# Optimization experiments

Hardware: AMD Instinct MI355X
Metric: run time of the kernel (lower is better)

## Reference

```python
import jax, jax.numpy as jnp
import numpy as np

H, KVH, HD, D, FF = 16, 4, 128, 2048, 7168
EPS = 1e-5
ROPE_THETA = 10000.0
SCALE_FACTOR, SCALE_GAP = 1.0, 0.7


def rms_norm(x, w):
    v = jnp.mean(jnp.square(x.astype(jnp.float32)), axis=-1, keepdims=True)
    return (x.astype(jnp.float32) * jax.lax.rsqrt(v + EPS)).astype(x.dtype) * w


def apply_rope(x, pos):
    # x: [B,S,h,HD], pos: [S]
    inv = 1.0 / (ROPE_THETA ** (jnp.arange(0, HD, 2, dtype=jnp.float32) / HD))
    ang = pos.astype(jnp.float32)[:, None] * inv[None, :]              # [S,HD/2]
    cos = jnp.concatenate([jnp.cos(ang)] * 2, -1)[None, :, None, :]    # [1,S,1,HD]
    sin = jnp.concatenate([jnp.sin(ang)] * 2, -1)[None, :, None, :]
    x1, x2 = jnp.split(x, 2, axis=-1)
    rot = jnp.concatenate([-x2, x1], axis=-1)
    return x * cos + rot * sin


def attention(x, q_w, k_w, v_w, o_w):
    B, S, _ = x.shape
    pos = jnp.arange(S)
    q = apply_rope((x @ q_w.T).reshape(B, S, H, HD), pos)
    k = apply_rope((x @ k_w.T).reshape(B, S, KVH, HD), pos)
    v = (x @ v_w.T).reshape(B, S, KVH, HD)
    rep = H // KVH
    k = jnp.repeat(k, rep, axis=2)   # [B,S,H,HD]
    v = jnp.repeat(v, rep, axis=2)
    scores = jnp.einsum('bqhd,bkhd->bhqk', q, k) / np.sqrt(HD).astype(np.float32)
    causal = jnp.tril(jnp.ones((S, S), dtype=bool))
    scores = jnp.where(causal[None, None], scores, jnp.finfo(scores.dtype).min)
    probs = jax.nn.softmax(scores, axis=-1)
    out = jnp.einsum('bhqk,bkhd->bqhd', probs, v).reshape(B, S, H * HD)
    return out @ o_w.T


def mlp(x, gate_w, up_w, down_w):
    return (jax.nn.silu(x @ gate_w.T) * (x @ up_w.T)) @ down_w.T


def setup_inputs() -> dict:
    key = jax.random.key(0)
    ks = jax.random.split(key, 12)
    B, S = 2, 2048
    w = lambda k, shp: (jax.random.normal(k, shp, dtype=jnp.float32) * 0.02)
    return {
        'hidden_states': jax.random.normal(ks[0], (B, S, D), dtype=jnp.float32),
        'topk_mask': jax.random.randint(ks[1], (B, S), 0, 2) > 0,
        'topk_scores': jax.random.uniform(ks[2], (B, S), dtype=jnp.float32),
        'ln1_w': jnp.ones((D,), jnp.float32),
        'ln2_w': jnp.ones((D,), jnp.float32),
        'q_w': w(ks[3], (H * HD, D)),
        'k_w': w(ks[4], (KVH * HD, D)),
        'v_w': w(ks[5], (KVH * HD, D)),
        'o_w': w(ks[6], (D, H * HD)),
        'gate_w': w(ks[7], (FF, D)),
        'up_w': w(ks[8], (FF, D)),
        'down_w': w(ks[9], (D, FF)),
    }


def reference(hidden_states, topk_mask, topk_scores, ln1_w, ln2_w,
              q_w, k_w, v_w, o_w, gate_w, up_w, down_w):
    # attention block
    h = hidden_states + attention(rms_norm(hidden_states, ln1_w), q_w, k_w, v_w, o_w)
    # MoD top-k masked MLP: only selected tokens go through MLP, scaled, scattered back
    m = mlp(rms_norm(h, ln2_w), gate_w, up_w, down_w)
    scores = 0.5 * SCALE_FACTOR + (topk_scores - 0.5) * SCALE_GAP
    upd = jnp.where(topk_mask[..., None], m * scores[..., None], 0.0)
    return h + upd
```

## Files before the change

### kernel.cpp

```cpp
#include <hip/hip_runtime.h>
#include <stdint.h>

#define SEQ    2048
#define DMODEL 2048
#define NTOK   4096
#define NHEAD  16
#define NKVH   4
#define HDIM   128
#define FFDIM  7168
#define FFH    3584
#define QKVS   3072

typedef __bf16 bf16x8 __attribute__((ext_vector_type(8)));
typedef float  floatx4 __attribute__((ext_vector_type(4)));

__device__ __forceinline__ float bf2f(unsigned short u) {
  union { unsigned int i; float f; } v; v.i = ((unsigned int)u) << 16; return v.f;
}
__device__ __forceinline__ unsigned short f2bf(float f) {
  union { float f; unsigned int u; } v; v.f = f;
  unsigned int r = (v.u + 0x7FFFu + ((v.u >> 16) & 1u)) >> 16;
  return (unsigned short)r;
}
__device__ __forceinline__ uint4 ld8f32(const float* p) {
  float4 a = *(const float4*)p, b = *(const float4*)(p + 4);
  union { unsigned short s[8]; uint4 v; } o;
  o.s[0] = f2bf(a.x); o.s[1] = f2bf(a.y); o.s[2] = f2bf(a.z); o.s[3] = f2bf(a.w);
  o.s[4] = f2bf(b.x); o.s[5] = f2bf(b.y); o.s[6] = f2bf(b.z); o.s[7] = f2bf(b.w);
  return o.v;
}

__device__ __forceinline__ void gload16(const unsigned short* g, unsigned short* l) {
  __builtin_amdgcn_global_load_lds(
      (const __attribute__((address_space(1))) unsigned int*)g,
      (__attribute__((address_space(3))) unsigned int*)l, 16, 0, 0);
}

__global__ __launch_bounds__(256) void wconv(const float* __restrict__ s,
                                             unsigned short* __restrict__ d) {
  const size_t i = ((size_t)blockIdx.x * 256 + threadIdx.x) * 8;
  *(uint4*)(d + i) = ld8f32(s + i);
}

__global__ __launch_bounds__(256) void wconv_dn(const float* __restrict__ s,
                                                unsigned short* __restrict__ d, int koff) {
  const int r = blockIdx.x;
  const float* sp = s + (size_t)r * FFDIM + koff;
  unsigned short* dp = d + (size_t)r * FFH;
  for (int c = threadIdx.x * 8; c < FFH; c += 2048)
    *(uint4*)(dp + c) = ld8f32(sp + c);
}

#define GEMM_CORE(Aptr, Wptr, KK)                                                \
  __shared__ __align__(16) unsigned short As[128 * 32];                          \
  __shared__ __align__(16) unsigned short Bs[128 * 32];                          \
  const int tid  = threadIdx.x;                                                  \
  const int wave = tid >> 6, lane = tid & 63;                                    \
  const int quad = lane >> 4, l16 = lane & 15;                                   \
  const int row0 = blockIdx.y * 128, col0 = blockIdx.x * 128;                    \
  const int wm = (wave >> 1) * 64, wn = (wave & 1) * 64;                         \
  const floatx4 z = {0.f, 0.f, 0.f, 0.f};                                       \
  floatx4 acc[4][4];                                                             \
  _Pragma("unroll") for (int i = 0; i < 4; ++i)                                  \
  _Pragma("unroll") for (int j = 0; j < 4; ++j) acc[i][j] = z;                   \
  const int ar0 = tid >> 2, ac0 = (tid & 3) << 3;                                \
  unsigned short* lA0 = &As[wave * 512];                                         \
  unsigned short* lA1 = &As[2048 + wave * 512];                                  \
  unsigned short* lB0 = &Bs[wave * 512];                                         \
  unsigned short* lB1 = &Bs[2048 + wave * 512];                                  \
  const unsigned short* gA0 = (Aptr) + (size_t)(row0 + ar0) * (KK) + ac0;        \
  const unsigned short* gA1 = (Aptr) + (size_t)(row0 + 64 + ar0) * (KK) + ac0;   \
  const unsigned short* gB0 = (Wptr) + (size_t)(col0 + ar0) * (KK) + ac0;        \
  const unsigned short* gB1 = (Wptr) + (size_t)(col0 + 64 + ar0) * (KK) + ac0;   \
  for (int k0 = 0; k0 < (KK); k0 += 32) {                                        \
    gload16(gA0 + k0, lA0);                                                      \
    gload16(gA1 + k0, lA1);                                                      \
    gload16(gB0 + k0, lB0);                                                      \
    gload16(gB1 + k0, lB1);                                                      \
    __syncthreads();                                                             \
    bf16x8 af[4], bfr[4];                                                        \
    _Pragma("unroll") for (int i = 0; i < 4; ++i) {                              \
      af[i]  = *(const bf16x8*)&As[(wm + i * 16 + l16) * 32 + quad * 8];         \
      bfr[i] = *(const bf16x8*)&Bs[(wn + i * 16 + l16) * 32 + quad * 8];         \
    }                                                                            \
    _Pragma("unroll") for (int mi = 0; mi < 4; ++mi)                             \
    _Pragma("unroll") for (int ni = 0; ni < 4; ++ni)                             \
      acc[mi][ni] =                                                              \
          __builtin_amdgcn_mfma_f32_16x16x32_bf16(af[mi], bfr[ni], acc[mi][ni], 0, 0, 0); \
    __syncthreads();                                                             \
  }

__global__ __launch_bounds__(256) void gemm_bt(
    const unsigned short* __restrict__ A, const unsigned short* __restrict__ W,
    unsigned short* __restrict__ C, int N, int K) {
  GEMM_CORE(A, W, K)
#pragma unroll
  for (int mi = 0; mi < 4; ++mi) {
    const int r = row0 + wm + mi * 16 + quad * 4;
#pragma unroll
    for (int ni = 0; ni < 4; ++ni) {
      const int cc = col0 + wn + ni * 16 + l16;
#pragma unroll
      for (int reg = 0; reg < 4; ++reg)
        C[(size_t)(r + reg) * N + cc] = f2bf(acc[mi][ni][reg]);
    }
  }
}

__global__ __launch_bounds__(256) void gemm_o_res(
    const unsigned short* __restrict__ A, const unsigned short* __restrict__ W,
    const float* __restrict__ X, float* __restrict__ Hout) {
  GEMM_CORE(A, W, DMODEL)
#pragma unroll
  for (int mi = 0; mi < 4; ++mi) {
    const int r = row0 + wm + mi * 16 + quad * 4;
#pragma unroll
    for (int ni = 0; ni < 4; ++ni) {
      const int cc = col0 + wn + ni * 16 + l16;
#pragma unroll
      for (int reg = 0; reg < 4; ++reg) {
        const size_t idx = (size_t)(r + reg) * DMODEL + cc;
        Hout[idx] = X[idx] + acc[mi][ni][reg];
      }
    }
  }
}

__global__ __launch_bounds__(256) void gemm_down_add(
    const unsigned short* __restrict__ A, const unsigned short* __restrict__ W,
    const float* __restrict__ ts, const int* __restrict__ tok_of,
    const int* __restrict__ cnt, float* __restrict__ out) {
  const int nrow = *cnt;
  if (blockIdx.y * 128 >= nrow) return;
  GEMM_CORE(A, W, FFH)
#pragma unroll
  for (int mi = 0; mi < 4; ++mi) {
    const int r = row0 + wm + mi * 16 + quad * 4;
#pragma unroll
    for (int ni = 0; ni < 4; ++ni) {
      const int cc = col0 + wn + ni * 16 + l16;
#pragma unroll
      for (int reg = 0; reg < 4; ++reg) {
        const int rr = r + reg;
        if (rr < nrow) {
          const int tok = tok_of[rr];
          const float scv = 0.5f + (ts[tok] - 0.5f) * 0.7f;
          out[(size_t)tok * DMODEL + cc] += acc[mi][ni][reg] * scv;
        }
      }
    }
  }
}

__global__ __launch_bounds__(256) void gemm_gateup(
    const unsigned short* __restrict__ A, const unsigned short* __restrict__ G,
    const unsigned short* __restrict__ U, const int* __restrict__ cnt,
    unsigned short* __restrict__ act) {
  if (blockIdx.y * 128 >= *cnt) return;
  __shared__ __align__(16) unsigned short As[128 * 32];
  __shared__ __align__(16) unsigned short Gs[64 * 32];
  __shared__ __align__(16) unsigned short Us[64 * 32];
  const int tid  = threadIdx.x;
  const int wave = tid >> 6, lane = tid & 63;
  const int quad = lane >> 4, l16 = lane & 15;
  const int row0 = blockIdx.y * 128, colg = blockIdx.x * 64;
  const int wm = (wave >> 1) * 64, wn = (wave & 1) * 32;

  const floatx4 z = {0.f, 0.f, 0.f, 0.f};
  floatx4 accG[4][2], accU[4][2];
#pragma unroll
  for (int i = 0; i < 4; ++i)
#pragma unroll
    for (int j = 0; j < 2; ++j) { accG[i][j] = z; accU[i][j] = z; }

  const int ar0 = tid >> 2, ac0 = (tid & 3) << 3;
  unsigned short* lA0 = &As[wave * 512];
  unsigned short* lA1 = &As[2048 + wave * 512];
  unsigned short* lG  = &Gs[wave * 512];
  unsigned short* lU  = &Us[wave * 512];
  const unsigned short* gA0 = A + (size_t)(row0 + ar0) * DMODEL + ac0;
  const unsigned short* gA1 = A + (size_t)(row0 + 64 + ar0) * DMODEL + ac0;
  const unsigned short* gG  = G + (size_t)(colg + ar0) * DMODEL + ac0;
  const unsigned short* gU  = U + (size_t)(colg + ar0) * DMODEL + ac0;

  for (int k0 = 0; k0 < DMODEL; k0 += 32) {
    gload16(gA0 + k0, lA0);
    gload16(gA1 + k0, lA1);
    gload16(gG + k0, lG);
    gload16(gU + k0, lU);
    __syncthreads();
    bf16x8 af[4], bg[2], bu[2];
#pragma unroll
    for (int i = 0; i < 4; ++i)
      af[i] = *(const bf16x8*)&As[(wm + i * 16 + l16) * 32 + quad * 8];
#pragma unroll
    for (int j = 0; j < 2; ++j) {
      bg[j] = *(const bf16x8*)&Gs[(wn + j * 16 + l16) * 32 + quad * 8];
      bu[j] = *(const bf16x8*)&Us[(wn + j * 16 + l16) * 32 + quad * 8];
    }
#pragma unroll
    for (int mi = 0; mi < 4; ++mi)
#pragma unroll
      for (int ni = 0; ni < 2; ++ni) {
        accG[mi][ni] = __builtin_amdgcn_mfma_f32_16x16x32_bf16(af[mi], bg[ni], accG[mi][ni], 0, 0, 0);
        accU[mi][ni] = __builtin_amdgcn_mfma_f32_16x16x32_bf16(af[mi], bu[ni], accU[mi][ni], 0, 0, 0);
      }
    __syncthreads();
  }
#pragma unroll
  for (int mi = 0; mi < 4; ++mi) {
    const int r = row0 + wm + mi * 16 + quad * 4;
#pragma unroll
    for (int ni = 0; ni < 2; ++ni) {
      const int cc = colg + wn + ni * 16 + l16;
#pragma unroll
      for (int reg = 0; reg < 4; ++reg) {
        const float g = accG[mi][ni][reg];
        const float u = accU[mi][ni][reg];
        const float s = g / (1.f + __expf(-g));
        act[(size_t)(r + reg) * FFH + cc] = f2bf(s * u);
      }
    }
  }
}

__global__ __launch_bounds__(256) void rmsnorm_f32(
    const float* __restrict__ x, const float* __restrict__ w,
    unsigned short* __restrict__ out) {
  __shared__ float red[4];
  const int row = blockIdx.x, tid = threadIdx.x;
  const int lane = tid & 63, wave = tid >> 6;
  const size_t base = (size_t)row * DMODEL + tid * 8;
  float4 a = *(const float4*)(x + base);
  float4 b = *(const float4*)(x + base + 4);
  float v[8] = {a.x, a.y, a.z, a.w, b.x, b.y, b.z, b.w};
  float ss = 0.f;
#pragma unroll
  for (int j = 0; j < 8; ++j) ss += v[j] * v[j];
#pragma unroll
  for (int off = 32; off; off >>= 1) ss += __shfl_xor(ss, off);
  if (lane == 0) red[wave] = ss;
  __syncthreads();
  const float tot = red[0] + red[1] + red[2] + red[3];
  const float rms = rsqrtf(tot * (1.f / (float)DMODEL) + 1e-5f);
  float4 wa = *(const float4*)(w + tid * 8);
  float4 wb = *(const float4*)(w + tid * 8 + 4);
  const float wv[8] = {wa.x, wa.y, wa.z, wa.w, wb.x, wb.y, wb.z, wb.w};
  unsigned short o[8];
#pragma unroll
  for (int j = 0; j < 8; ++j) o[j] = f2bf(v[j] * rms * wv[j]);
  *(uint4*)(out + base) = *(const uint4*)o;
}

__global__ void zero_cnt(int* cnt) { *cnt = 0; }

__global__ __launch_bounds__(256) void rms_gather(
    const float* __restrict__ x, const float* __restrict__ w,
    const int* __restrict__ mask, int* __restrict__ cnt,
    int* __restrict__ tok_of, unsigned short* __restrict__ xc) {
  const int row = blockIdx.x;
  if (!mask[row]) return;
  __shared__ float red[4];
  __shared__ int ppos;
  const int tid = threadIdx.x, lane = tid & 63, wave = tid >> 6;
  if (tid == 0) { const int p = atomicAdd(cnt, 1); ppos = p; tok_of[p] = row; }
  const size_t base = (size_t)row * DMODEL + tid * 8;
  float4 a = *(const float4*)(x + base);
  float4 b = *(const float4*)(x + base + 4);
  float v[8] = {a.x, a.y, a.z, a.w, b.x, b.y, b.z, b.w};
  float ss = 0.f;
#pragma unroll
  for (int j = 0; j < 8; ++j) ss += v[j] * v[j];
#pragma unroll
  for (int off = 32; off; off >>= 1) ss += __shfl_xor(ss, off);
  if (lane == 0) red[wave] = ss;
  __syncthreads();
  const float tot = red[0] + red[1] + red[2] + red[3];
  const float rms = rsqrtf(tot * (1.f / (float)DMODEL) + 1e-5f);
  float4 wa = *(const float4*)(w + tid * 8);
  float4 wb = *(const float4*)(w + tid * 8 + 4);
  const float wv[8] = {wa.x, wa.y, wa.z, wa.w, wb.x, wb.y, wb.z, wb.w};
  unsigned short o[8];
#pragma unroll
  for (int j = 0; j < 8; ++j) o[j] = f2bf(v[j] * rms * wv[j]);
  *(uint4*)(xc + (size_t)ppos * DMODEL + tid * 8) = *(const uint4*)o;
}

__global__ __launch_bounds__(256) void rope_k(unsigned short* __restrict__ buf,
                                              int nh, int rstride) {
  const int t = blockIdx.x;
  const int s = t & (SEQ - 1);
  const int d = threadIdx.x & 63;
  const float inv = __expf((float)d * -0.14391156843712787f);
  float sn, cs;
  __sincosf((float)s * inv, &sn, &cs);
  const int npair = nh * 64;
  for (int idx = threadIdx.x; idx < npair; idx += 256) {
    const int hh = idx >> 6;
    unsigned short* p = buf + (size_t)t * rstride + hh * 128 + d;
    const float x1 = bf2f(p[0]), x2 = bf2f(p[64]);
    p[0]  = f2bf(x1 * cs - x2 * sn);
    p[64] = f2bf(x2 * cs + x1 * sn);
  }
}

__global__ __launch_bounds__(512, 2) void attn(
    const unsigned short* __restrict__ QKV,
    unsigned short* __restrict__ O) {
  __shared__ __align__(16) unsigned short Ks[64 * 136];
  __shared__ __align__(16) unsigned short Vt[128 * 80];
  __shared__ __align__(16) unsigned short Ps[8][16 * 88];
  const int h = blockIdx.x, b = blockIdx.z;
  const int qtL = blockIdx.y, qtH = 15 - qtL;
  const int kvh = h >> 2;
  const int tid = threadIdx.x, wave = tid >> 6, lane = tid & 63;
  const int quad = lane >> 4, l16 = lane & 15;
  const int wloH = qtH * 128 + wave * 16;
  const int wloL = qtL * 128 + wave * 16;
  const int qrH = wloH + quad * 4, qrL = wloL + quad * 4;
  const float sscale = 0.08838834764831845f;

  bf16x8 qfH[4], qfL[4];
  {
    const unsigned short* qpH =
        QKV + (size_t)(b * SEQ + wloH + l16) * QKVS + h * HDIM + quad * 8;
    const unsigned short* qpL =
        QKV + (size_t)(b * SEQ + wloL + l16) * QKVS + h * HDIM + quad * 8;
#pragma unroll
    for (int c = 0; c < 4; ++c) {
      qfH[c] = *(const bf16x8*)(qpH + 32 * c);
      qfL[c] = *(const bf16x8*)(qpL + 32 * c);
    }
  }
  const floatx4 z = {0.f, 0.f, 0.f, 0.f};
  floatx4 accH[8], accL[8];
#pragma unroll
  for (int i = 0; i < 8; ++i) { accH[i] = z; accL[i] = z; }
  float mH[4], lH[4], mL[4], lL[4];
#pragma unroll
  for (int r = 0; r < 4; ++r) { mH[r] = -1e30f; lH[r] = 0.f; mL[r] = -1e30f; lL[r] = 0.f; }

  const int sr = tid >> 4, scol = (tid & 15) * 8;
  const unsigned short* kvb = QKV + (size_t)(b * SEQ) * QKVS + kvh * HDIM;
  uint4 kreg[2], vreg[2];

  auto LOADT = [&](int t0) {
#pragma unroll
    for (int it = 0; it < 2; ++it) {
      const int r = sr + it * 32;
      kreg[it] = *(const uint4*)(kvb + (size_t)(t0 + r) * QKVS + 2048 + scol);
      vreg[it] = *(const uint4*)(kvb + (size_t)(t0 + r) * QKVS + 2560 + scol);
    }
  };
  auto STORET = [&]() {
#pragma unroll
    for (int it = 0; it < 2; ++it) {
      const int r = sr + it * 32;
      *(uint4*)&Ks[r * 136 + scol] = kreg[it];
      const unsigned short* dv = (const unsigned short*)&vreg[it];
      const int tb = r >> 3, pos = r & 7;
#pragma unroll
      for (int j = 0; j < 8; ++j) {
        const int d = scol + j;
        const int sb = tb ^ ((d >> 3) & 7);
        Vt[d * 80 + sb * 8 + pos] = dv[j];
      }
    }
  };

  auto COMPUTE = [&](const bf16x8* qf, floatx4* accO, float* mrow, float* lrow,
                     int qrowC, int wlo, int t0) {
    floatx4 sc[4];
    __builtin_amdgcn_s_setprio(1);
#pragma unroll
    for (int ni = 0; ni < 4; ++ni) {
      floatx4 s = z;
#pragma unroll
      for (int c = 0; c < 4; ++c) {
        bf16x8 kf = *(const bf16x8*)&Ks[(ni * 16 + l16) * 136 + c * 32 + quad * 8];
        s = __builtin_amdgcn_mfma_f32_16x16x32_bf16(qf[c], kf, s, 0, 0, 0);
      }
      sc[ni] = s;
    }
    __builtin_amdgcn_s_setprio(0);

    if (t0 + 63 > wlo) {
#pragma unroll
      for (int ni = 0; ni < 4; ++ni) {
        const int kcol = t0 + ni * 16 + l16;
#pragma unroll
        for (int reg = 0; reg < 4; ++reg) {
          const float vv = sc[ni][reg] * sscale;
          sc[ni][reg] = (kcol > qrowC + reg) ? -1e30f : vv;
        }
      }
    } else {
#pragma unroll
      for (int ni = 0; ni < 4; ++ni)
#pragma unroll
        for (int reg = 0; reg < 4; ++reg) sc[ni][reg] *= sscale;
    }

    float mx[4];
#pragma unroll
    for (int reg = 0; reg < 4; ++reg) {
      float m0 = fmaxf(fmaxf(sc[0][reg], sc[1][reg]), fmaxf(sc[2][reg], sc[3][reg]));
#pragma unroll
      for (int off = 1; off < 16; off <<= 1) m0 = fmaxf(m0, __shfl_xor(m0, off));
      mx[reg] = m0;
    }
    const bool grow = (mx[0] > mrow[0] + 8.f) || (mx[1] > mrow[1] + 8.f) ||
                      (mx[2] > mrow[2] + 8.f) || (mx[3] > mrow[3] + 8.f);
    if (__any(grow)) {
#pragma unroll
      for (int reg = 0; reg < 4; ++reg) {
        const float mnew = fmaxf(mrow[reg], mx[reg]);
        const float alpha = __expf(mrow[reg] - mnew);
        mrow[reg] = mnew;
        lrow[reg] *= alpha;
#pragma unroll
        for (int nd = 0; nd < 8; ++nd) accO[nd][reg] *= alpha;
      }
    }
#pragma unroll
    for (int reg = 0; reg < 4; ++reg) {
      float rs = 0.f;
#pragma unroll
      for (int ni = 0; ni < 4; ++ni) {
        const float p = __expf(sc[ni][reg] - mrow[reg]);
        sc[ni][reg] = p;
        rs += p;
      }
#pragma unroll
      for (int off = 1; off < 16; off <<= 1) rs += __shfl_xor(rs, off);
      lrow[reg] += rs;
    }
#pragma unroll
    for (int ni = 0; ni < 4; ++ni)
#pragma unroll
      for (int reg = 0; reg < 4; ++reg)
        Ps[wave][(quad * 4 + reg) * 88 + ni * 16 + l16] = f2bf(sc[ni][reg]);
    const bf16x8 pa0 = *(const bf16x8*)&Ps[wave][l16 * 88 + quad * 8];
    const bf16x8 pa1 = *(const bf16x8*)&Ps[wave][l16 * 88 + 32 + quad * 8];
    __builtin_amdgcn_s_setprio(1);
#pragma unroll
    for (int nd = 0; nd < 8; ++nd) {
      const int d = nd * 16 + l16;
      const int f = (d >> 3) & 7;
      bf16x8 v0 = *(const bf16x8*)&Vt[d * 80 + ((quad ^ f) << 3)];
      bf16x8 v1 = *(const bf16x8*)&Vt[d * 80 + (((quad + 4) ^ f) << 3)];
      accO[nd] = __builtin_amdgcn_mfma_f32_16x16x32_bf16(pa0, v0, accO[nd], 0, 0, 0);
      accO[nd] = __builtin_amdgcn_mfma_f32_16x16x32_bf16(pa1, v1, accO[nd], 0, 0, 0);
    }
    __builtin_amdgcn_s_setprio(0);
  };

  const int ntL = 2 * qtL + 2, ntH = 2 * qtH + 2;
  LOADT(0);
  STORET();
  __syncthreads();

  for (int ti = 0; ti < ntH; ++ti) {
    const int t0 = ti * 64;
    const bool more = (ti + 1 < ntH);
    if (more) LOADT(t0 + 64);

    if (t0 <= wloH + 15) COMPUTE(qfH, accH, mH, lH, qrH, wloH, t0);
    if (ti < ntL && t0 <= wloL + 15) COMPUTE(qfL, accL, mL, lL, qrL, wloL, t0);

    __syncthreads();
    if (more) {
      STORET();
      __syncthreads();
    }
  }
#pragma unroll
  for (int nd = 0; nd < 8; ++nd)
#pragma unroll
    for (int reg = 0; reg < 4; ++reg) {
      const float oH = accH[nd][reg] / lH[reg];
      O[(size_t)(b * SEQ + qrH + reg) * (NHEAD * HDIM) + h * HDIM + nd * 16 + l16] = f2bf(oH);
      const float oL = accL[nd][reg] / lL[reg];
      O[(size_t)(b * SEQ + qrL + reg) * (NHEAD * HDIM) + h * HDIM + nd * 16 + l16] = f2bf(oL);
    }
}

extern "C" void kernel_launch(void* const* d_in, const int* in_sizes, int n_in,
                              void* d_out, int out_size, void* d_ws, size_t ws_size,
                              hipStream_t stream) {
  (void)in_sizes; (void)n_in; (void)out_size; (void)ws_size;
  const float* x    = (const float*)d_in[0];
  const int*   mask = (const int*)d_in[1];
  const float* ts   = (const float*)d_in[2];
  const float* ln1  = (const float*)d_in[3];
  const float* ln2  = (const float*)d_in[4];
  const float* q_w  = (const float*)d_in[5];
  const float* k_w  = (const float*)d_in[6];
  const float* v_w  = (const float*)d_in[7];
  const float* o_w  = (const float*)d_in[8];
  const float* g_w  = (const float*)d_in[9];
  const float* u_w  = (const float*)d_in[10];
  const float* dn_w = (const float*)d_in[11];
  float* out = (float*)d_out;

  char* ws = (char*)d_ws;
  unsigned short* xn    = (unsigned short*)(ws + 0);
  unsigned short* qkv   = (unsigned short*)(ws + 16777216);
  unsigned short* wqkv  = (unsigned short*)(ws + 41943040);
  unsigned short* attno = (unsigned short*)(ws + 41943040);
  unsigned short* wo    = (unsigned short*)(ws + 58720256);
  unsigned short* xc    = (unsigned short*)(ws + 0);
  unsigned short* wg    = (unsigned short*)(ws + 16777216);
  unsigned short* wu    = (unsigned short*)(ws + 31457280);
  unsigned short* wdn   = (unsigned short*)(ws + 16777216);
  unsigned short* act   = (unsigned short*)(ws + 46137344);
  int*            cnt   = (int*)           (ws + 75497472);
  int*            tok_of= (int*)           (ws + 75501568);

  wconv<<<2048, 256, 0, stream>>>(q_w, wqkv);
  wconv<<<512,  256, 0, stream>>>(k_w, wqkv + (size_t)2048 * DMODEL);
  wconv<<<512,  256, 0, stream>>>(v_w, wqkv + (size_t)2560 * DMODEL);
  wconv<<<2048, 256, 0, stream>>>(o_w, wo);

  rmsnorm_f32<<<NTOK, 256, 0, stream>>>(x, ln1, xn);
  gemm_bt<<<dim3(QKVS / 128, 32), 256, 0, stream>>>(xn, wqkv, qkv, QKVS, 2048);
  rope_k<<<NTOK, 256, 0, stream>>>(qkv, 20, QKVS);
  attn<<<dim3(NHEAD, 8, 2), 512, 0, stream>>>(qkv, attno);
  gemm_o_res<<<dim3(16, 32), 256, 0, stream>>>(attno, wo, x, out);

  zero_cnt<<<1, 1, 0, stream>>>(cnt);
  rms_gather<<<NTOK, 256, 0, stream>>>(out, ln2, mask, cnt, tok_of, xc);
  for (int hf = 0; hf < 2; ++hf) {
    wconv<<<3584, 256, 0, stream>>>(g_w + (size_t)hf * FFH * DMODEL, wg);
    wconv<<<3584, 256, 0, stream>>>(u_w + (size_t)hf * FFH * DMODEL, wu);
    gemm_gateup<<<dim3(FFH / 64, 32), 256, 0, stream>>>(xc, wg, wu, cnt, act);
    wconv_dn<<<2048, 256, 0, stream>>>(dn_w, wdn, hf * FFH);
    gemm_down_add<<<dim3(16, 32), 256, 0, stream>>>(act, wdn, ts, tok_of, cnt, out);
  }
}
```

Measured before the change: 942.0 us.

## Split down-proj K with atomics, shrink attention tiles, fuse weight conversion launches

Result: slower. 1.031 ms (+9.4%).

```diff
diff --git a/kernel.cpp b/kernel.cpp
--- a/kernel.cpp
+++ b/kernel.cpp
@@ -36,10 +36,31 @@
       (__attribute__((address_space(3))) unsigned int*)l, 16, 0, 0);
 }
 
-__global__ __launch_bounds__(256) void wconv(const float* __restrict__ s,
-                                             unsigned short* __restrict__ d) {
-  const size_t i = ((size_t)blockIdx.x * 256 + threadIdx.x) * 8;
-  *(uint4*)(d + i) = ld8f32(s + i);
+__global__ __launch_bounds__(256) void wconv_attn(
+    const float* __restrict__ q, const float* __restrict__ k,
+    const float* __restrict__ v, const float* __restrict__ o,
+    unsigned short* __restrict__ wqkv, unsigned short* __restrict__ wo,
+    int* __restrict__ cnt) {
+  if (blockIdx.x == 0 && threadIdx.x == 0) *cnt = 0;
+  const int r = blockIdx.x;
+  const float* src;
+  unsigned short* dst;
+  if (r < 2048)      { src = q + (size_t)r * DMODEL;          dst = wqkv + (size_t)r * DMODEL; }
+  else if (r < 2560) { src = k + (size_t)(r - 2048) * DMODEL; dst = wqkv + (size_t)r * DMODEL; }
+  else if (r < 3072) { src = v + (size_t)(r - 2560) * DMODEL; dst = wqkv + (size_t)r * DMODEL; }
+  else               { src = o + (size_t)(r - 3072) * DMODEL; dst = wo + (size_t)(r - 3072) * DMODEL; }
+  const int c = threadIdx.x * 8;
+  *(uint4*)(dst + c) = ld8f32(src + c);
+}
+
+__global__ __launch_bounds__(256) void wconv_gu(
+    const float* __restrict__ g, const float* __restrict__ u,
+    unsigned short* __restrict__ dst, int hf) {
+  const int r = blockIdx.x;
+  const float* src = (r < FFH) ? g + ((size_t)hf * FFH + r) * DMODEL
+                               : u + ((size_t)hf * FFH + (r - FFH)) * DMODEL;
+  const int c = threadIdx.x * 8;
+  *(uint4*)(dst + (size_t)r * DMODEL + c) = ld8f32(src + c);
 }
 
 __global__ __launch_bounds__(256) void wconv_dn(const float* __restrict__ s,
@@ -51,7 +72,7 @@
     *(uint4*)(dp + c) = ld8f32(sp + c);
 }
 
-#define GEMM_CORE(Aptr, Wptr, KK)                                                \
+#define GEMM_CORE_G(Aptr, Wptr, LDA, LDB, KLEN, KOFF)                            \
   __shared__ __align__(16) unsigned short As[128 * 32];                          \
   __shared__ __align__(16) unsigned short Bs[128 * 32];                          \
   const int tid  = threadIdx.x;                                                  \
@@ -68,11 +89,11 @@
   unsigned short* lA1 = &As[2048 + wave * 512];                                  \
   unsigned short* lB0 = &Bs[wave * 512];                                         \
   unsigned short* lB1 = &Bs[2048 + wave * 512];                                  \
-  const unsigned short* gA0 = (Aptr) + (size_t)(row0 + ar0) * (KK) + ac0;        \
-  const unsigned short* gA1 = (Aptr) + (size_t)(row0 + 64 + ar0) * (KK) + ac0;   \
-  const unsigned short* gB0 = (Wptr) + (size_t)(col0 + ar0) * (KK) + ac0;        \
-  const unsigned short* gB1 = (Wptr) + (size_t)(col0 + 64 + ar0) * (KK) + ac0;   \
-  for (int k0 = 0; k0 < (KK); k0 += 32) {                                        \
+  const unsigned short* gA0 = (Aptr) + (size_t)(row0 + ar0) * (LDA) + (KOFF) + ac0;      \
+  const unsigned short* gA1 = (Aptr) + (size_t)(row0 + 64 + ar0) * (LDA) + (KOFF) + ac0; \
+  const unsigned short* gB0 = (Wptr) + (size_t)(col0 + ar0) * (LDB) + (KOFF) + ac0;      \
+  const unsigned short* gB1 = (Wptr) + (size_t)(col0 + 64 + ar0) * (LDB) + (KOFF) + ac0; \
+  for (int k0 = 0; k0 < (KLEN); k0 += 32) {                                      \
     gload16(gA0 + k0, lA0);                                                      \
     gload16(gA1 + k0, lA1);                                                      \
     gload16(gB0 + k0, lB0);                                                      \
@@ -93,7 +114,7 @@
 __global__ __launch_bounds__(256) void gemm_bt(
     const unsigned short* __restrict__ A, const unsigned short* __restrict__ W,
     unsigned short* __restrict__ C, int N, int K) {
-  GEMM_CORE(A, W, K)
+  GEMM_CORE_G(A, W, K, K, K, 0)
 #pragma unroll
   for (int mi = 0; mi < 4; ++mi) {
     const int r = row0 + wm + mi * 16 + quad * 4;
@@ -110,7 +131,7 @@
 __global__ __launch_bounds__(256) void gemm_o_res(
     const unsigned short* __restrict__ A, const unsigned short* __restrict__ W,
     const float* __restrict__ X, float* __restrict__ Hout) {
-  GEMM_CORE(A, W, DMODEL)
+  GEMM_CORE_G(A, W, DMODEL, DMODEL, DMODEL, 0)
 #pragma unroll
   for (int mi = 0; mi < 4; ++mi) {
     const int r = row0 + wm + mi * 16 + quad * 4;
@@ -132,7 +153,8 @@
     const int* __restrict__ cnt, float* __restrict__ out) {
   const int nrow = *cnt;
   if (blockIdx.y * 128 >= nrow) return;
-  GEMM_CORE(A, W, FFH)
+  const int koff = blockIdx.z * (FFH / 2);
+  GEMM_CORE_G(A, W, FFH, FFH, FFH / 2, koff)
 #pragma unroll
   for (int mi = 0; mi < 4; ++mi) {
     const int r = row0 + wm + mi * 16 + quad * 4;
@@ -145,7 +167,7 @@
         if (rr < nrow) {
           const int tok = tok_of[rr];
           const float scv = 0.5f + (ts[tok] - 0.5f) * 0.7f;
-          out[(size_t)tok * DMODEL + cc] += acc[mi][ni][reg] * scv;
+          atomicAdd(out + (size_t)tok * DMODEL + cc, acc[mi][ni][reg] * scv);
         }
       }
     }
@@ -251,8 +273,6 @@
   for (int j = 0; j < 8; ++j) o[j] = f2bf(v[j] * rms * wv[j]);
   *(uint4*)(out + base) = *(const uint4*)o;
 }
-
-__global__ void zero_cnt(int* cnt) { *cnt = 0; }
 
 __global__ __launch_bounds__(256) void rms_gather(
     const float* __restrict__ x, const float* __restrict__ w,
@@ -304,19 +324,19 @@
   }
 }
 
-__global__ __launch_bounds__(512, 2) void attn(
+__global__ __launch_bounds__(256, 2) void attn(
     const unsigned short* __restrict__ QKV,
     unsigned short* __restrict__ O) {
   __shared__ __align__(16) unsigned short Ks[64 * 136];
   __shared__ __align__(16) unsigned short Vt[128 * 80];
-  __shared__ __align__(16) unsigned short Ps[8][16 * 88];
+  __shared__ __align__(16) unsigned short Ps[4][16 * 88];
   const int h = blockIdx.x, b = blockIdx.z;
-  const int qtL = blockIdx.y, qtH = 15 - qtL;
+  const int qtL = blockIdx.y, qtH = 31 - qtL;
   const int kvh = h >> 2;
   const int tid = threadIdx.x, wave = tid >> 6, lane = tid & 63;
   const int quad = lane >> 4, l16 = lane & 15;
-  const int wloH = qtH * 128 + wave * 16;
-  const int wloL = qtL * 128 + wave * 16;
+  const int wloH = qtH * 64 + wave * 16;
+  const int wloL = qtL * 64 + wave * 16;
   const int qrH = wloH + quad * 4, qrL = wloL + quad * 4;
   const float sscale = 0.08838834764831845f;
 
@@ -342,20 +362,20 @@
 
   const int sr = tid >> 4, scol = (tid & 15) * 8;
   const unsigned short* kvb = QKV + (size_t)(b * SEQ) * QKVS + kvh * HDIM;
-  uint4 kreg[2], vreg[2];
+  uint4 kreg[4], vreg[4];
 
   auto LOADT = [&](int t0) {
 #pragma unroll
-    for (int it = 0; it < 2; ++it) {
-      const int r = sr + it * 32;
+    for (int it = 0; it < 4; ++it) {
+      const int r = sr + it * 16;
       kreg[it] = *(const uint4*)(kvb + (size_t)(t0 + r) * QKVS + 2048 + scol);
       vreg[it] = *(const uint4*)(kvb + (size_t)(t0 + r) * QKVS + 2560 + scol);
     }
   };
   auto STORET = [&]() {
 #pragma unroll
-    for (int it = 0; it < 2; ++it) {
-      const int r = sr + it * 32;
+    for (int it = 0; it < 4; ++it) {
+      const int r = sr + it * 16;
       *(uint4*)&Ks[r * 136 + scol] = kreg[it];
       const unsigned short* dv = (const unsigned short*)&vreg[it];
       const int tb = r >> 3, pos = r & 7;
@@ -455,7 +475,7 @@
     __builtin_amdgcn_s_setprio(0);
   };
 
-  const int ntL = 2 * qtL + 2, ntH = 2 * qtH + 2;
+  const int ntL = qtL + 1, ntH = qtH + 1;
   LOADT(0);
   STORET();
   __syncthreads();
@@ -465,8 +485,8 @@
     const bool more = (ti + 1 < ntH);
     if (more) LOADT(t0 + 64);
 
-    if (t0 <= wloH + 15) COMPUTE(qfH, accH, mH, lH, qrH, wloH, t0);
-    if (ti < ntL && t0 <= wloL + 15) COMPUTE(qfL, accL, mL, lL, qrL, wloL, t0);
+    COMPUTE(qfH, accH, mH, lH, qrH, wloH, t0);
+    if (ti < ntL) COMPUTE(qfL, accL, mL, lL, qrL, wloL, t0);
 
     __syncthreads();
     if (more) {
@@ -517,24 +537,18 @@
   int*            cnt   = (int*)           (ws + 75497472);
   int*            tok_of= (int*)           (ws + 75501568);
 
-  wconv<<<2048, 256, 0, stream>>>(q_w, wqkv);
-  wconv<<<512,  256, 0, stream>>>(k_w, wqkv + (size_t)2048 * DMODEL);
-  wconv<<<512,  256, 0, stream>>>(v_w, wqkv + (size_t)2560 * DMODEL);
-  wconv<<<2048, 256, 0, stream>>>(o_w, wo);
-
+  wconv_attn<<<5120, 256, 0, stream>>>(q_w, k_w, v_w, o_w, wqkv, wo, cnt);
   rmsnorm_f32<<<NTOK, 256, 0, stream>>>(x, ln1, xn);
   gemm_bt<<<dim3(QKVS / 128, 32), 256, 0, stream>>>(xn, wqkv, qkv, QKVS, 2048);
   rope_k<<<NTOK, 256, 0, stream>>>(qkv, 20, QKVS);
-  attn<<<dim3(NHEAD, 8, 2), 512, 0, stream>>>(qkv, attno);
+  attn<<<dim3(NHEAD, 16, 2), 256, 0, stream>>>(qkv, attno);
   gemm_o_res<<<dim3(16, 32), 256, 0, stream>>>(attno, wo, x, out);
 
-  zero_cnt<<<1, 1, 0, stream>>>(cnt);
   rms_gather<<<NTOK, 256, 0, stream>>>(out, ln2, mask, cnt, tok_of, xc);
   for (int hf = 0; hf < 2; ++hf) {
-    wconv<<<3584, 256, 0, stream>>>(g_w + (size_t)hf * FFH * DMODEL, wg);
-    wconv<<<3584, 256, 0, stream>>>(u_w + (size_t)hf * FFH * DMODEL, wu);
+    wconv_gu<<<2 * FFH, 256, 0, stream>>>(g_w, u_w, wg, hf);
     gemm_gateup<<<dim3(FFH / 64, 32), 256, 0, stream>>>(xc, wg, wu, cnt, act);
     wconv_dn<<<2048, 256, 0, stream>>>(dn_w, wdn, hf * FFH);
-    gemm_down_add<<<dim3(16, 32), 256, 0, stream>>>(act, wdn, ts, tok_of, cnt, out);
-  }
-}
+    gemm_down_add<<<dim3(16, 32, 2), 256, 0, stream>>>(act, wdn, ts, tok_of, cnt, out);
+  }
+}
```
